# Kernel tuning notes

Hardware: AMD Instinct MI355X
Metric: run time of the kernel (lower is better)

Reference implementation:

```python
import jax, jax.numpy as jnp
import numpy as np

B, S, D, H = 2, 2048, 1024, 16
DK = D // H  # 64


def setup_inputs() -> dict:
    key = jax.random.key(0)
    ks = jax.random.split(key, 10)
    query = jax.random.normal(ks[0], (B, S, D), dtype=jnp.float32)
    key_t = jax.random.normal(ks[1], (B, S, D), dtype=jnp.float32)
    value = jax.random.normal(ks[2], (B, S, D), dtype=jnp.float32)
    # binary mask [batch, q_size, k_size]: causal lower-triangular, same per batch
    mask = jnp.broadcast_to(jnp.tril(jnp.ones((S, S), dtype=jnp.float32)), (B, S, S))
    sc = 0.02
    Wq = jax.random.normal(ks[3], (D, D), dtype=jnp.float32) * sc
    bq = jnp.zeros((D,), dtype=jnp.float32)
    Wk = jax.random.normal(ks[4], (D, D), dtype=jnp.float32) * sc
    bk = jnp.zeros((D,), dtype=jnp.float32)
    Wv = jax.random.normal(ks[5], (D, D), dtype=jnp.float32) * sc
    bv = jnp.zeros((D,), dtype=jnp.float32)
    return {"query": query, "key": key_t, "value": value, "mask": mask,
            "Wq": Wq, "bq": bq, "Wk": Wk, "bk": bk, "Wv": Wv, "bv": bv}


def reference(query, key, value, mask, Wq, bq, Wk, bk, Wv, bv):
    # ReLU-activated Q/K/V projections (Dense(..., activation='relu'))
    Q = jax.nn.relu(query @ Wq + bq)   # [B, Sq, D]
    K = jax.nn.relu(key @ Wk + bk)     # [B, Sk, D]
    V = jax.nn.relu(value @ Wv + bv)   # [B, Sk, D]
    b, sq, _ = Q.shape
    sk = K.shape[1]
    # split-concat head trick == reshape last dim into (H, DK) heads
    Qh = Q.reshape(b, sq, H, DK)
    Kh = K.reshape(b, sk, H, DK)
    Vh = V.reshape(b, sk, H, DK)
    scores = jnp.einsum('bqhd,bkhd->bhqk', Qh, Kh) / jnp.sqrt(jnp.float32(DK))
    m = mask[:, None, :, :]  # broadcast over heads (mask_expander tiles over h)
    scores = scores * m + (1.0 - m) * (-1e10)
    attn = jax.nn.softmax(scores, axis=-1)  # dropout is a no-op (see notes)
    out = jnp.einsum('bhqk,bkhd->bqhd', attn, Vh).reshape(b, sq, H * DK)
    return out
```

## Files before the change

kernel.cpp:

```cpp
#include <hip/hip_runtime.h>
#include <hip/hip_bf16.h>

#define B_  2
#define S_  2048
#define D_  1024
#define H_  16
#define DK_ 64
#define NR  (B_*S_)
#define QT_ 16
#define CPP 20

typedef __bf16 bf16_t;
typedef __attribute__((ext_vector_type(8)))  __bf16 bf16x8;
typedef __attribute__((ext_vector_type(4)))  float  f32x4;
typedef __attribute__((ext_vector_type(16))) float  f32x16;

#define QSCALE (0.125f * 1.44269504088896340736f)

__device__ inline void gl_lds16(const void* g, void* l) {
  __builtin_amdgcn_global_load_lds(
      (const __attribute__((address_space(1))) void*)g,
      (__attribute__((address_space(3))) void*)l, 16, 0, 0);
}

__device__ inline unsigned pack2(float a, float b) {
  union { bf16_t h[2]; unsigned u; } x;
  x.h[0] = (bf16_t)a; x.h[1] = (bf16_t)b;
  return x.u;
}

__device__ inline bf16x8 frag(const bf16_t* p, int r, int j) {
  return *(const bf16x8*)(p + r * 64 + ((j ^ (r & 7)) * 8));
}

__device__ const unsigned char ord_p[CPP] = {7,6,5,4,3,2,7,6,5,4,7,6,1,7,5,3,6,4,2,0};
__device__ const unsigned char ord_c[CPP] = {0,0,0,0,0,0,1,1,1,1,2,2,0,3,2,1,3,2,1,0};
__device__ const unsigned char cbase[8]   = {0,1,2,4,6,9,12,16};

__global__ void cvt_fp32_bf16(const float* __restrict__ xq, const float* __restrict__ xk,
                              const float* __restrict__ xv,
                              bf16_t* __restrict__ yq, bf16_t* __restrict__ yk,
                              bf16_t* __restrict__ yv) {
  const int z = blockIdx.y;
  const float* x = z == 0 ? xq : z == 1 ? xk : xv;
  bf16_t*      y = z == 0 ? yq : z == 1 ? yk : yv;
  size_t i = ((size_t)blockIdx.x * 256 + threadIdx.x) * 8;
  float4 a = *(const float4*)(x + i);
  float4 b = *(const float4*)(x + i + 4);
  union { bf16_t h[8]; uint4 u; } o;
  o.h[0] = (bf16_t)a.x; o.h[1] = (bf16_t)a.y; o.h[2] = (bf16_t)a.z; o.h[3] = (bf16_t)a.w;
  o.h[4] = (bf16_t)b.x; o.h[5] = (bf16_t)b.y; o.h[6] = (bf16_t)b.z; o.h[7] = (bf16_t)b.w;
  *(uint4*)(y + i) = o.u;
}

__global__ void transpose_cvt(const float* __restrict__ wq, const float* __restrict__ wk,
                              const float* __restrict__ wv,
                              bf16_t* __restrict__ oq, bf16_t* __restrict__ ok,
                              bf16_t* __restrict__ ov) {
  const int z = blockIdx.z;
  const float* W = z == 0 ? wq : z == 1 ? wk : wv;
  bf16_t*     WT = z == 0 ? oq : z == 1 ? ok : ov;
  __shared__ float t[32][33];
  int x  = blockIdx.x * 32 + threadIdx.x;
  int y0 = blockIdx.y * 32;
  for (int i = threadIdx.y; i < 32; i += 8)
    t[i][threadIdx.x] = W[(size_t)(y0 + i) * D_ + x];
  __syncthreads();
  int k  = y0 + threadIdx.x;
  int n0 = blockIdx.x * 32;
  for (int i = threadIdx.y; i < 32; i += 8)
    WT[(size_t)(n0 + i) * D_ + k] = (bf16_t)t[threadIdx.x][i];
}

__global__ __launch_bounds__(256, 2) void gemm_qkv(
    const bf16_t* __restrict__ Xq, const bf16_t* __restrict__ Xk, const bf16_t* __restrict__ Xv,
    const bf16_t* __restrict__ Wq, const bf16_t* __restrict__ Wk, const bf16_t* __restrict__ Wv,
    const float* __restrict__ bq, const float* __restrict__ bk, const float* __restrict__ bv,
    bf16_t* __restrict__ Yq, bf16_t* __restrict__ Yk, bf16_t* __restrict__ Yv)
{
  const int z = blockIdx.z;
  const bf16_t* X    = z == 0 ? Xq : z == 1 ? Xk : Xv;
  const bf16_t* WT   = z == 0 ? Wq : z == 1 ? Wk : Wv;
  const float*  bias = z == 0 ? bq : z == 1 ? bk : bv;
  bf16_t*       Y    = z == 0 ? Yq : z == 1 ? Yk : Yv;
  const float scale  = z == 0 ? QSCALE : 1.0f;
  const int transposedV = (z == 2);

  __shared__ bf16_t As[128 * 64];
  __shared__ bf16_t Bs[128 * 64];
  const int m0 = blockIdx.x * 128, n0 = blockIdx.y * 128;
  const int t = threadIdx.x, l = t & 63, w = t >> 6;
  const int wm = (w & 1) * 64, wn = (w >> 1) * 64;
  const int lr = l & 15, lg4 = l >> 4;

  f32x4 acc[4][4] = {};

  for (int k0 = 0; k0 < D_; k0 += 64) {
    #pragma unroll
    for (int i = 0; i < 4; i++) {
      int c = i * 256 + t;
      int row = c >> 3, j0 = c & 7;
      int sc = (j0 ^ (row & 7)) * 8;
      gl_lds16(X  + (size_t)(m0 + row) * D_ + k0 + sc, As + c * 8);
      gl_lds16(WT + (size_t)(n0 + row) * D_ + k0 + sc, Bs + c * 8);
    }
    __syncthreads();

    #pragma unroll
    for (int kk = 0; kk < 2; kk++) {
      const int j = kk * 4 + lg4;
      bf16x8 af[4], bfr[4];
      #pragma unroll
      for (int mf = 0; mf < 4; mf++)
        af[mf] = frag(As, wm + mf * 16 + lr, j);
      #pragma unroll
      for (int nf = 0; nf < 4; nf++)
        bfr[nf] = frag(Bs, wn + nf * 16 + lr, j);
      #pragma unroll
      for (int mf = 0; mf < 4; mf++)
        #pragma unroll
        for (int nf = 0; nf < 4; nf++)
          acc[mf][nf] = __builtin_amdgcn_mfma_f32_16x16x32_bf16(
              af[mf], bfr[nf], acc[mf][nf], 0, 0, 0);
    }
    __syncthreads();
  }

  #pragma unroll
  for (int nf = 0; nf < 4; nf++) {
    int col = n0 + wn + nf * 16 + lr;
    float bvv = bias[col];
    #pragma unroll
    for (int mf = 0; mf < 4; mf++) {
      #pragma unroll
      for (int r = 0; r < 4; r++) {
        int row = m0 + wm + mf * 16 + lg4 * 4 + r;
        float v = fmaxf(acc[mf][nf][r] + bvv, 0.f) * scale;
        if (!transposedV) {
          Y[(size_t)row * D_ + col] = (bf16_t)v;
        } else {
          int bb = row >> 11, s = row & (S_ - 1);
          int hh = col >> 6,  dk = col & (DK_ - 1);
          Y[(((size_t)(bb * H_ + hh)) * DK_ + dk) * S_ + s] = (bf16_t)v;
        }
      }
    }
  }
}

__device__ inline void qkt(const bf16_t* kl, const bf16x8* qf, int lq, int hh,
                           f32x16& s0, f32x16& s1) {
  #pragma unroll
  for (int s = 0; s < 4; s++) {
    bf16x8 k0 = frag(kl, lq, 2 * s + hh);
    bf16x8 k1 = frag(kl, lq + 32, 2 * s + hh);
    s0 = __builtin_amdgcn_mfma_f32_32x32x16_bf16(k0, qf[s], s0, 0, 0, 0);
    s1 = __builtin_amdgcn_mfma_f32_32x32x16_bf16(k1, qf[s], s1, 0, 0, 0);
  }
}

__device__ inline void cmask(f32x16& s0, f32x16& s1, int kb, int q, int hh) {
  #pragma unroll
  for (int r = 0; r < 16; r++) {
    int krow = kb + (r & 3) + 8 * (r >> 2) + 4 * hh;
    if (krow > q)      s0[r] = -1e30f;
    if (krow + 32 > q) s1[r] = -1e30f;
  }
}

__device__ inline void pv_quad(const f32x16& p0, const f32x16& p1,
                               const bf16_t* vl, int lq, int hh,
                               f32x16& o0, f32x16& o1) {
  #pragma unroll
  for (int st = 0; st < 4; st++) {
    const f32x16& ps = (st < 2) ? p0 : p1;
    const int bb = (st & 1) * 8;
    unsigned lo0 = pack2(ps[bb + 0], ps[bb + 1]), lo1 = pack2(ps[bb + 2], ps[bb + 3]);
    unsigned hi0 = pack2(ps[bb + 4], ps[bb + 5]), hi1 = pack2(ps[bb + 6], ps[bb + 7]);
    unsigned sA = hh ? lo0 : hi0, sB = hh ? lo1 : hi1;
    unsigned rA = __shfl_xor(sA, 32, 64), rB = __shfl_xor(sB, 32, 64);
    union { unsigned u[4]; bf16x8 v; } pf;
    pf.u[0] = hh ? rA : lo0;  pf.u[1] = hh ? rB : lo1;
    pf.u[2] = hh ? hi0 : rA;  pf.u[3] = hh ? hi1 : rB;
    bf16x8 v0 = frag(vl, lq, 2 * st + hh);
    bf16x8 v1 = frag(vl, lq + 32, 2 * st + hh);
    o0 = __builtin_amdgcn_mfma_f32_32x32x16_bf16(v0, pf.v, o0, 0, 0, 0);
    o1 = __builtin_amdgcn_mfma_f32_32x32x16_bf16(v1, pf.v, o1, 0, 0, 0);
  }
}

__global__ __launch_bounds__(512, 4) void attn_fwd(
    const bf16_t* __restrict__ Q, const bf16_t* __restrict__ K,
    const bf16_t* __restrict__ VT, bf16_t* __restrict__ PO,
    float* __restrict__ PL)
{
  __shared__ bf16_t lbuf[3][8192];

  const int bx = blockIdx.x;
  const int unit = bx >> 5, bh = bx & 31;
  const int p_ = ord_p[unit], ch = ord_c[unit];
  const int b = bh >> 4, h = bh & 15;
  const int kt0 = ch * 8;
  const int nt = min(8, (4 * p_ + 4) - kt0);
  const int slotbase = (bh * CPP + cbase[p_] + ch) * 2;

  const int t = threadIdx.x, w = t >> 6, l = t & 63;
  const int u = w >> 2, w4 = w & 3;
  const int qt = 2 * p_ + u;
  const int q0 = qt * 128 + w4 * 32;
  const int lq = l & 31, hh = l >> 5;
  const int qq = q0 + lq;
  const int nfull = 2 * qt + (w4 >> 1);

  const bf16_t* Qb = Q  + ((size_t)(b * S_ + qq)) * D_ + h * DK_;
  const bf16_t* Kb = K  + ((size_t)b * S_) * D_ + h * DK_;
  const bf16_t* Vb = VT + ((size_t)(b * H_ + h)) * ((size_t)DK_ * S_);

  const int r0 = t >> 3, j0 = t & 7;
  const int jx = (j0 ^ (r0 & 7)) * 8;

  #define STAGE_TILE(bi, kt_) do {                                    \
    const int kb_ = (kt_) << 6;                                       \
    bf16_t* Lb = lbuf[bi];                                            \
    gl_lds16(Kb + (size_t)(kb_ + r0) * D_ + jx, Lb + t * 8);          \
    gl_lds16(Vb + (size_t)r0 * S_ + kb_ + jx,   Lb + 4096 + t * 8);   \
  } while (0)

  bf16x8 qf[4];
  #pragma unroll
  for (int s = 0; s < 4; s++)
    qf[s] = *(const bf16x8*)(Qb + s * 16 + hh * 8);
  asm volatile("s_waitcnt vmcnt(0)" ::: "memory");
  #pragma unroll
  for (int s = 0; s < 4; s++)
    asm volatile("" : "+v"(qf[s]));

  f32x16 o0 = {}, o1 = {};
  f32x16 lacc = {};

  STAGE_TILE(0, kt0);
  STAGE_TILE(1, kt0 + 1);
  asm volatile("s_waitcnt vmcnt(2)" ::: "memory");
  __builtin_amdgcn_s_barrier();
  __builtin_amdgcn_sched_barrier(0);

  for (int p = 0; p < nt; ++p) {
    const int kt = kt0 + p;
    const int cur = p - (p / 3) * 3;

    if (p + 2 < nt) {
      const int nb = (p + 2) - ((p + 2) / 3) * 3;
      STAGE_TILE(nb, kt + 2);
    }

    if (kt <= nfull) {
      const bf16_t* kl = lbuf[cur];
      const bf16_t* vl = lbuf[cur] + 4096;

      f32x16 s0 = {}, s1 = {};
      __builtin_amdgcn_s_setprio(1);
      qkt(kl, qf, lq, hh, s0, s1);
      __builtin_amdgcn_s_setprio(0);
      if (kt == nfull) cmask(s0, s1, kt << 6, qq, hh);

      f32x16 p0, p1;
      #pragma unroll
      for (int r2 = 0; r2 < 16; r2++) {
        p0[r2] = exp2f(s0[r2]);
        p1[r2] = exp2f(s1[r2]);
        lacc[r2] += p0[r2] + p1[r2];
      }

      __builtin_amdgcn_s_setprio(1);
      pv_quad(p0, p1, vl, lq, hh, o0, o1);
      __builtin_amdgcn_s_setprio(0);
    }

    if (p + 1 < nt) {
      if (p + 2 < nt) asm volatile("s_waitcnt vmcnt(2)" ::: "memory");
      else            asm volatile("s_waitcnt vmcnt(0)" ::: "memory");
      __builtin_amdgcn_s_barrier();
      __builtin_amdgcn_sched_barrier(0);
    }
  }
  #undef STAGE_TILE

  float lrun = 0.f;
  #pragma unroll
  for (int r2 = 0; r2 < 16; r2++) lrun += lacc[r2];
  lrun += __shfl_xor(lrun, 32, 64);

  bf16_t* po = PO + (size_t)(slotbase + u) * 8192;
  #pragma unroll
  for (int r2 = 0; r2 < 16; r2++) {
    int dk = (r2 & 3) + 8 * (r2 >> 2) + 4 * hh;
    po[dk * 128 + w4 * 32 + lq]        = (bf16_t)o0[r2];
    po[(dk + 32) * 128 + w4 * 32 + lq] = (bf16_t)o1[r2];
  }
  if (hh == 0)
    PL[(size_t)(slotbase + u) * 128 + w4 * 32 + lq] = lrun;
}

__global__ __launch_bounds__(256, 4) void attn_combine(
    const bf16_t* __restrict__ PO, const float* __restrict__ PL,
    float* __restrict__ out)
{
  const int bx = blockIdx.x;
  const int b = bx >> 8, h = (bx >> 4) & 15, qt = bx & 15;
  const int bh = b * H_ + h;
  const int p_ = qt >> 1, u = qt & 1;
  const int nc = (p_ >> 1) + 1;
  const int slot0 = (bh * CPP + cbase[p_]) * 2 + u;

  __shared__ float ls[64][132];
  __shared__ float inv[128];

  const int t = threadIdx.x;

  float acc[4][8];
  #pragma unroll
  for (int i = 0; i < 4; i++)
    #pragma unroll
    for (int j = 0; j < 8; j++) acc[i][j] = 0.f;

  for (int c = 0; c < nc; ++c) {
    const bf16_t* po = PO + (size_t)(slot0 + 2 * c) * 8192;
    #pragma unroll
    for (int i = 0; i < 4; i++) {
      bf16x8 v = *(const bf16x8*)(po + i * 2048 + t * 8);
      #pragma unroll
      for (int j = 0; j < 8; j++) acc[i][j] += (float)v[j];
    }
  }

  if (t < 128) {
    float s = 0.f;
    for (int c = 0; c < nc; ++c) s += PL[(size_t)(slot0 + 2 * c) * 128 + t];
    inv[t] = 1.0f / s;
  }

  #pragma unroll
  for (int i = 0; i < 4; i++)
    #pragma unroll
    for (int j = 0; j < 8; j++)
      ls[(t >> 4) + 16 * i][(t & 15) * 8 + j] = acc[i][j];
  __syncthreads();

  const int q = t >> 1, c0 = (t & 1) * 32;
  const float iv = inv[q];
  float* op = out + ((size_t)(b * S_ + qt * 128 + q)) * D_ + h * DK_ + c0;
  #pragma unroll
  for (int v = 0; v < 8; v++) {
    float4 x = { ls[c0 + 4 * v][q] * iv,     ls[c0 + 4 * v + 1][q] * iv,
                 ls[c0 + 4 * v + 2][q] * iv, ls[c0 + 4 * v + 3][q] * iv };
    *(float4*)(op + 4 * v) = x;
  }
}

extern "C" void kernel_launch(void* const* d_in, const int* in_sizes, int n_in,
                              void* d_out, int out_size, void* d_ws, size_t ws_size,
                              hipStream_t stream) {
  const float* query = (const float*)d_in[0];
  const float* keyi  = (const float*)d_in[1];
  const float* val   = (const float*)d_in[2];
  const float* Wq = (const float*)d_in[4];
  const float* bq = (const float*)d_in[5];
  const float* Wk = (const float*)d_in[6];
  const float* bk = (const float*)d_in[7];
  const float* Wv = (const float*)d_in[8];
  const float* bv = (const float*)d_in[9];
  float* out = (float*)d_out;

  const size_t XB = (size_t)NR * D_;
  const size_t WB = (size_t)D_ * D_;
  bf16_t* ws  = (bf16_t*)d_ws;
  bf16_t* Xq  = ws;
  bf16_t* Xk  = Xq  + XB;
  bf16_t* Xv  = Xk  + XB;
  bf16_t* WTq = Xv  + XB;
  bf16_t* WTk = WTq + WB;
  bf16_t* WTv = WTk + WB;
  bf16_t* Qm  = WTv + WB;
  bf16_t* Km  = Qm  + XB;
  bf16_t* VTm = Km  + XB;
  bf16_t* PO  = ws;
  float*  PL  = (float*)((char*)d_ws + 22u * 1024 * 1024);

  dim3 cgrid(XB / (256 * 8), 3);
  cvt_fp32_bf16<<<cgrid, 256, 0, stream>>>(query, keyi, val, Xq, Xk, Xv);

  dim3 tgrid(D_ / 32, D_ / 32, 3), tblk(32, 8);
  transpose_cvt<<<tgrid, tblk, 0, stream>>>(Wq, Wk, Wv, WTq, WTk, WTv);

  dim3 ggrid(NR / 128, D_ / 128, 3);
  gemm_qkv<<<ggrid, 256, 0, stream>>>(Xq, Xk, Xv, WTq, WTk, WTv,
                                      bq, bk, bv, Qm, Km, VTm);

  attn_fwd<<<dim3(32 * CPP), 512, 0, stream>>>(Qm, Km, VTm, PO, PL);
  attn_combine<<<dim3(B_ * H_ * QT_), 256, 0, stream>>>(PO, PL, out);
}
```

Measured before the change: 115.4 us.

## Process key tiles in pairs with double-buffered LDS to halve barriers

```diff
diff --git a/kernel.cpp b/kernel.cpp
--- a/kernel.cpp
+++ b/kernel.cpp
@@ -194,7 +194,7 @@
     const bf16_t* __restrict__ VT, bf16_t* __restrict__ PO,
     float* __restrict__ PL)
 {
-  __shared__ bf16_t lbuf[3][8192];
+  __shared__ bf16_t lbuf[2][16384];
 
   const int bx = blockIdx.x;
   const int unit = bx >> 5, bh = bx & 31;
@@ -202,6 +202,7 @@
   const int b = bh >> 4, h = bh & 15;
   const int kt0 = ch * 8;
   const int nt = min(8, (4 * p_ + 4) - kt0);
+  const int np = nt >> 1;
   const int slotbase = (bh * CPP + cbase[p_] + ch) * 2;
 
   const int t = threadIdx.x, w = t >> 6, l = t & 63;
@@ -219,11 +220,13 @@
   const int r0 = t >> 3, j0 = t & 7;
   const int jx = (j0 ^ (r0 & 7)) * 8;
 
-  #define STAGE_TILE(bi, kt_) do {                                    \
-    const int kb_ = (kt_) << 6;                                       \
-    bf16_t* Lb = lbuf[bi];                                            \
-    gl_lds16(Kb + (size_t)(kb_ + r0) * D_ + jx, Lb + t * 8);          \
-    gl_lds16(Vb + (size_t)r0 * S_ + kb_ + jx,   Lb + 4096 + t * 8);   \
+  #define STAGE_PAIR(bi, kt_) do {                                        \
+    const int kb_ = (kt_) << 6;                                           \
+    bf16_t* Lb = lbuf[bi];                                                \
+    gl_lds16(Kb + (size_t)(kb_ + r0) * D_ + jx,      Lb + t * 8);         \
+    gl_lds16(Kb + (size_t)(kb_ + 64 + r0) * D_ + jx, Lb + 4096 + t * 8);  \
+    gl_lds16(Vb + (size_t)r0 * S_ + kb_ + jx,        Lb + 8192 + t * 8);  \
+    gl_lds16(Vb + (size_t)r0 * S_ + kb_ + 64 + jx,   Lb + 12288 + t * 8); \
   } while (0)
 
   bf16x8 qf[4];
@@ -238,52 +241,72 @@
   f32x16 o0 = {}, o1 = {};
   f32x16 lacc = {};
 
-  STAGE_TILE(0, kt0);
-  STAGE_TILE(1, kt0 + 1);
-  asm volatile("s_waitcnt vmcnt(2)" ::: "memory");
+  STAGE_PAIR(0, kt0);
+  asm volatile("s_waitcnt vmcnt(0)" ::: "memory");
   __builtin_amdgcn_s_barrier();
   __builtin_amdgcn_sched_barrier(0);
 
-  for (int p = 0; p < nt; ++p) {
-    const int kt = kt0 + p;
-    const int cur = p - (p / 3) * 3;
-
-    if (p + 2 < nt) {
-      const int nb = (p + 2) - ((p + 2) / 3) * 3;
-      STAGE_TILE(nb, kt + 2);
-    }
-
-    if (kt <= nfull) {
-      const bf16_t* kl = lbuf[cur];
-      const bf16_t* vl = lbuf[cur] + 4096;
-
-      f32x16 s0 = {}, s1 = {};
+  for (int p = 0; p < np; ++p) {
+    const int t0 = kt0 + 2 * p, t1 = t0 + 1;
+    const int cur = p & 1;
+
+    if (p + 1 < np) STAGE_PAIR(cur ^ 1, t0 + 2);
+
+    const bf16_t* base = lbuf[cur];
+    if (t1 <= nfull) {
+      f32x16 sa0 = {}, sa1 = {}, sb0 = {}, sb1 = {};
       __builtin_amdgcn_s_setprio(1);
-      qkt(kl, qf, lq, hh, s0, s1);
+      qkt(base,        qf, lq, hh, sa0, sa1);
+      qkt(base + 4096, qf, lq, hh, sb0, sb1);
       __builtin_amdgcn_s_setprio(0);
-      if (kt == nfull) cmask(s0, s1, kt << 6, qq, hh);
-
-      f32x16 p0, p1;
+      if (t1 == nfull) cmask(sb0, sb1, t1 << 6, qq, hh);
+
+      f32x16 pa0, pa1;
       #pragma unroll
       for (int r2 = 0; r2 < 16; r2++) {
-        p0[r2] = exp2f(s0[r2]);
-        p1[r2] = exp2f(s1[r2]);
-        lacc[r2] += p0[r2] + p1[r2];
+        pa0[r2] = exp2f(sa0[r2]);
+        pa1[r2] = exp2f(sa1[r2]);
+        lacc[r2] += pa0[r2] + pa1[r2];
       }
-
       __builtin_amdgcn_s_setprio(1);
-      pv_quad(p0, p1, vl, lq, hh, o0, o1);
+      pv_quad(pa0, pa1, base + 8192, lq, hh, o0, o1);
       __builtin_amdgcn_s_setprio(0);
-    }
-
-    if (p + 1 < nt) {
-      if (p + 2 < nt) asm volatile("s_waitcnt vmcnt(2)" ::: "memory");
-      else            asm volatile("s_waitcnt vmcnt(0)" ::: "memory");
+
+      f32x16 pb0, pb1;
+      #pragma unroll
+      for (int r2 = 0; r2 < 16; r2++) {
+        pb0[r2] = exp2f(sb0[r2]);
+        pb1[r2] = exp2f(sb1[r2]);
+        lacc[r2] += pb0[r2] + pb1[r2];
+      }
+      __builtin_amdgcn_s_setprio(1);
+      pv_quad(pb0, pb1, base + 12288, lq, hh, o0, o1);
+      __builtin_amdgcn_s_setprio(0);
+    } else if (t0 <= nfull) {
+      f32x16 sa0 = {}, sa1 = {};
+      __builtin_amdgcn_s_setprio(1);
+      qkt(base, qf, lq, hh, sa0, sa1);
+      __builtin_amdgcn_s_setprio(0);
+      cmask(sa0, sa1, t0 << 6, qq, hh);
+      f32x16 pa0, pa1;
+      #pragma unroll
+      for (int r2 = 0; r2 < 16; r2++) {
+        pa0[r2] = exp2f(sa0[r2]);
+        pa1[r2] = exp2f(sa1[r2]);
+        lacc[r2] += pa0[r2] + pa1[r2];
+      }
+      __builtin_amdgcn_s_setprio(1);
+      pv_quad(pa0, pa1, base + 8192, lq, hh, o0, o1);
+      __builtin_amdgcn_s_setprio(0);
+    }
+
+    if (p + 1 < np) {
+      asm volatile("s_waitcnt vmcnt(0)" ::: "memory");
       __builtin_amdgcn_s_barrier();
       __builtin_amdgcn_sched_barrier(0);
     }
   }
-  #undef STAGE_TILE
+  #undef STAGE_PAIR
 
   float lrun = 0.f;
   #pragma unroll
```

New measurement: 166.9 us. 44.7% more time.
